# Kernel tuning notes

Measured on AMD Instinct MI355X. Metric: run time of the kernel, lower is better.

Reference implementation:

```python
import jax, jax.numpy as jnp
import numpy as np

BN_EPS = 1e-5
DIST_EPS = 1e-8


def setup_inputs() -> dict:
    key = jax.random.key(0)
    ks = jax.random.split(key, 8)
    B, N, S = 8, 8192, 2048
    D_unk, D_kn = 128, 256
    inp = {
        "unknown_xyz": jax.random.uniform(ks[0], (B, N, 3), dtype=jnp.float32),
        "known_xyz": jax.random.uniform(ks[1], (B, S, 3), dtype=jnp.float32),
        "unknown_points": jax.random.normal(ks[2], (B, N, D_unk), dtype=jnp.float32),
        "known_points": jax.random.normal(ks[3], (B, S, D_kn), dtype=jnp.float32),
        "W0": jax.random.normal(ks[4], (256, 384), dtype=jnp.float32) * (1.0 / np.sqrt(384)),
        "b0": jnp.zeros((256,), jnp.float32),
        "g0": jnp.ones((256,), jnp.float32),
        "beta0": jnp.zeros((256,), jnp.float32),
        "W1": jax.random.normal(ks[5], (128, 256), dtype=jnp.float32) * (1.0 / np.sqrt(256)),
        "b1": jnp.zeros((128,), jnp.float32),
        "g1": jnp.ones((128,), jnp.float32),
        "beta1": jnp.zeros((128,), jnp.float32),
    }
    return inp


def _three_nn(unknown_xyz, known_xyz):
    # squared pairwise distances [B, N, S]
    d = jnp.sum((unknown_xyz[:, :, None, :] - known_xyz[:, None, :, :]) ** 2, axis=-1)
    neg_top, idx = jax.lax.top_k(-d, 3)  # 3 smallest distances
    return -neg_top, idx  # dists [B,N,3], idx [B,N,3]


def _conv_bn_relu(x, W, b, g, beta):
    # x: [B, N, Cin]; 1x1 Conv1d == per-point linear
    y = jnp.einsum("bnc,oc->bno", x, W) + b
    mean = jnp.mean(y, axis=(0, 1))
    var = jnp.var(y, axis=(0, 1))  # biased, as BatchNorm training forward
    y = g * (y - mean) * jax.lax.rsqrt(var + BN_EPS) + beta
    return jax.nn.relu(y)


def reference(unknown_xyz, known_xyz, unknown_points, known_points,
              W0, b0, g0, beta0, W1, b1, g1, beta1):
    dists, idx = _three_nn(unknown_xyz, known_xyz)
    dist_recip = 1.0 / (dists + DIST_EPS)
    weight = dist_recip / jnp.sum(dist_recip, axis=2, keepdims=True)  # [B,N,3]
    # gather 3 neighbor features: [B,N,3,D_kn]
    gathered = jax.vmap(lambda f, i: f[i])(known_points, idx)
    interpolated = jnp.sum(weight[..., None] * gathered, axis=2)  # [B,N,D_kn]
    x = jnp.concatenate([unknown_points, interpolated], axis=-1)  # [B,N,384]
    x = _conv_bn_relu(x, W0, b0, g0, beta0)
    x = _conv_bn_relu(x, W1, b1, g1, beta1)
    return x  # [B, N, 128]
```

## Files before the change

kernel.cpp:

```cpp
#include <hip/hip_runtime.h>
#include <hip/hip_bf16.h>


typedef __attribute__((ext_vector_type(8))) short short8;
typedef __attribute__((ext_vector_type(4))) float f32x4;

#define BB 8
#define NN 8192
#define SS 2048
#define M_TOT (BB * NN)
#define N1DIM 256
#define K2DIM 256
#define N2DIM 128
#define NCH 8
#define CHS (SS / NCH)
#define BK 64

#define KEY_MASK 0xFFFFF800u
#define IDX_MASK 0x7FFu

__device__ __forceinline__ unsigned short f2bf(float f) {
    unsigned int x = __float_as_uint(f);
    unsigned int r = x + 0x7fffu + ((x >> 16) & 1u);
    return (unsigned short)(r >> 16);
}
__device__ __forceinline__ float bf2f(unsigned short u) {
    return __uint_as_float(((unsigned int)u) << 16);
}
__device__ __forceinline__ unsigned int med3_u32(unsigned int a, unsigned int b,
                                                 unsigned int c) {
    unsigned int r;
    asm("v_med3_u32 %0, %1, %2, %3" : "=v"(r) : "v"(a), "v"(b), "v"(c));
    return r;
}

__device__ __forceinline__ void gload_lds16(const void* g, void* lds) {
    __builtin_amdgcn_global_load_lds(
        (const __attribute__((address_space(1))) unsigned int*)g,
        (__attribute__((address_space(3))) unsigned int*)lds, 16, 0, 0);
}

__global__ __launch_bounds__(256) void nn_cand_kernel(
    const float* __restrict__ uxyz,
    const float4* __restrict__ kpack,
    unsigned int* __restrict__ cand)
{
    const int tid  = threadIdx.x;
    const int bid  = blockIdx.x;
    const int ch   = bid & 7;
    const int tile = (bid >> 3) & 31;
    const int b    = bid >> 8;

    const int n = tile * 256 + tid;
    const float* up = uxyz + ((size_t)b * NN + n) * 3;
    const float ux = up[0], uy = up[1], uz = up[2];
    const float uu  = fmaf(ux, ux, fmaf(uy, uy, uz * uz));
    const float m2x = -2.0f * ux, m2y = -2.0f * uy, m2z = -2.0f * uz;

    const float4* kb = kpack + (size_t)b * SS + ch * CHS;
    const int base = ch * CHS;

    unsigned int k0 = 0xFFFFFFFFu, k1 = 0xFFFFFFFFu, k2 = 0xFFFFFFFFu;
#pragma unroll 8
    for (int s = 0; s < CHS; ++s) {
        float4 kc = kb[s];
        float d = kc.w + uu;
        d = fmaf(m2z, kc.z, d);
        d = fmaf(m2y, kc.y, d);
        d = fmaf(m2x, kc.x, d);
        d = fmaxf(d, 0.0f);
        unsigned int key = (__float_as_uint(d) & KEY_MASK) | (unsigned int)(base + s);
        unsigned int nk1 = med3_u32(k0, k1, key);
        unsigned int nk2 = med3_u32(k1, k2, key);
        k0 = min(k0, key);
        k1 = nk1;
        k2 = nk2;
    }

    const size_t pt = (size_t)b * NN + n;
    cand[(size_t)(ch * 3 + 0) * M_TOT + pt] = k0;
    cand[(size_t)(ch * 3 + 1) * M_TOT + pt] = k1;
    cand[(size_t)(ch * 3 + 2) * M_TOT + pt] = k2;
}

__global__ __launch_bounds__(256) void cvt_w_kernel(
    const float* __restrict__ W0, const float* __restrict__ W1,
    const float* __restrict__ kxyz,
    unsigned short* __restrict__ Wa, unsigned short* __restrict__ Wb,
    unsigned short* __restrict__ Wb1, float4* __restrict__ kpack,
    float* __restrict__ statsF)
{
    int i = blockIdx.x * 256 + threadIdx.x;
    if (blockIdx.x == 0) {
        for (int j = threadIdx.x; j < 768; j += 256) statsF[j] = 0.0f;
    }
    if (i < 256 * 384) {
        int o = i / 384, c = i - o * 384;
        unsigned short v = f2bf(W0[i]);
        if (c < 128) Wa[o * 128 + c] = v;
        else         Wb[o * 256 + (c - 128)] = v;
    }
    if (i < N2DIM * K2DIM) Wb1[i] = f2bf(W1[i]);
    if (i < BB * SS) {
        const float* p = kxyz + (size_t)i * 3;
        float px = p[0], py = p[1], pz = p[2];
        kpack[i] = make_float4(px, py, pz, fmaf(px, px, fmaf(py, py, pz * pz)));
    }
}

__global__ __launch_bounds__(512, 4) void zgemm_kernel(
    const float* __restrict__ kpts,
    const unsigned short* __restrict__ Wb,
    unsigned short* __restrict__ Z)
{
    __shared__ __align__(128) unsigned char smem[2 * 32768];

    const int tid = threadIdx.x;
    const int l = tid & 63, w = tid >> 6;
    const int wm = w >> 2, wn = w & 3;
    const int mt = blockIdx.x >> 1, nh = blockIdx.x & 1;
    const int row0 = mt * 128;
    const int srow = l >> 3, sbo = (l & 7) * 16;
    const int lr = tid >> 2, lcq = tid & 3;

    f32x4 acc[4][2];
#pragma unroll
    for (int m = 0; m < 4; ++m)
#pragma unroll
        for (int n = 0; n < 2; ++n) {
            f32x4 z = {0.f, 0.f, 0.f, 0.f};
            acc[m][n] = z;
        }

    const unsigned char* Bb = (const unsigned char*)Wb + (size_t)nh * 128 * 512;
    float4 af0, af1, af2, af3;

    auto issueA = [&](int t) {
        const float* src = kpts + (size_t)(row0 + lr) * 256 + t * 64 + lcq * 16;
        af0 = ((const float4*)src)[0];
        af1 = ((const float4*)src)[1];
        af2 = ((const float4*)src)[2];
        af3 = ((const float4*)src)[3];
    };
    auto stageB = [&](int buf, int t) {
        unsigned char* Bl = smem + buf * 32768 + 16384;
#pragma unroll
        for (int i = 0; i < 2; ++i) {
            const int r = w * 16 + i * 8 + srow;
            gload_lds16(Bb + (size_t)r * 512 + t * 128 + (sbo ^ ((r & 7) << 4)),
                        Bl + r * 128 + sbo);
        }
    };
    auto xformA = [&](int buf) {
        unsigned char* Al = smem + buf * 32768;
        short8 o0, o1;
        o0[0] = (short)f2bf(af0.x); o0[1] = (short)f2bf(af0.y);
        o0[2] = (short)f2bf(af0.z); o0[3] = (short)f2bf(af0.w);
        o0[4] = (short)f2bf(af1.x); o0[5] = (short)f2bf(af1.y);
        o0[6] = (short)f2bf(af1.z); o0[7] = (short)f2bf(af1.w);
        o1[0] = (short)f2bf(af2.x); o1[1] = (short)f2bf(af2.y);
        o1[2] = (short)f2bf(af2.z); o1[3] = (short)f2bf(af2.w);
        o1[4] = (short)f2bf(af3.x); o1[5] = (short)f2bf(af3.y);
        o1[6] = (short)f2bf(af3.z); o1[7] = (short)f2bf(af3.w);
        const int bo = lcq * 32;
        *(short8*)(Al + lr * 128 + ((bo) ^ ((lr & 7) << 4))) = o0;
        *(short8*)(Al + lr * 128 + ((bo + 16) ^ ((lr & 7) << 4))) = o1;
    };
    auto compute = [&](int buf) {
        const unsigned char* Al = smem + buf * 32768;
        const unsigned char* Bl = Al + 16384;
#pragma unroll
        for (int ks = 0; ks < 2; ++ks) {
            const int bo = ks * 64 + (l >> 4) * 16;
            short8 a[4], bq[2];
#pragma unroll
            for (int m = 0; m < 4; ++m) {
                const int r = wm * 64 + m * 16 + (l & 15);
                a[m] = *(const short8*)(Al + r * 128 + (bo ^ ((r & 7) << 4)));
            }
#pragma unroll
            for (int n = 0; n < 2; ++n) {
                const int r = wn * 32 + n * 16 + (l & 15);
                bq[n] = *(const short8*)(Bl + r * 128 + (bo ^ ((r & 7) << 4)));
            }
#pragma unroll
            for (int m = 0; m < 4; ++m)
#pragma unroll
                for (int n = 0; n < 2; ++n)
                    acc[m][n] = __builtin_amdgcn_mfma_f32_16x16x32_bf16(
                        a[m], bq[n], acc[m][n], 0, 0, 0);
        }
    };

    issueA(0);
    stageB(0, 0);
    xformA(0);
    __syncthreads();
#pragma unroll
    for (int t = 0; t < 4; ++t) {
        const int cur = t & 1;
        if (t + 1 < 4) { issueA(t + 1); stageB(cur ^ 1, t + 1); }
        compute(cur);
        if (t + 1 < 4) xformA(cur ^ 1);
        __syncthreads();
    }

#pragma unroll
    for (int m = 0; m < 4; ++m) {
        const int row = row0 + wm * 64 + m * 16 + (l >> 4) * 4;
#pragma unroll
        for (int n = 0; n < 2; ++n) {
            const int col = nh * 128 + wn * 32 + n * 16 + (l & 15);
            f32x4 v = acc[m][n];
#pragma unroll
            for (int r = 0; r < 4; ++r)
                Z[(size_t)(row + r) * 256 + col] = f2bf(v[r]);
        }
    }
}

__global__ __launch_bounds__(256) void merge_interp_z_kernel(
    const unsigned int* __restrict__ cand,
    const float4* __restrict__ kpack,
    const float* __restrict__ uxyz,
    const unsigned short* __restrict__ Z,
    unsigned short* __restrict__ xz)
{
    __shared__ int   sidx[64][3];
    __shared__ float sw[64][3];

    const int tid = threadIdx.x;
    const int bid = blockIdx.x;
    const int b   = bid & 7;
    const int pn  = (bid >> 3) * 64;

    if (tid < 64) {
        const size_t pt = (size_t)b * NN + pn + tid;

        unsigned int k[6];
#pragma unroll
        for (int i = 0; i < 6; ++i) k[i] = 0xFFFFFFFFu;
#pragma unroll
        for (int ch = 0; ch < NCH; ++ch) {
#pragma unroll
            for (int j = 0; j < 3; ++j) {
                unsigned int t = cand[(size_t)(ch * 3 + j) * M_TOT + pt];
#pragma unroll
                for (int i = 0; i < 6; ++i) {
                    unsigned int a = min(k[i], t);
                    t = max(k[i], t);
                    k[i] = a;
                }
            }
        }

        const float* up = uxyz + pt * 3;
        const float ux = up[0], uy = up[1], uz = up[2];
        const float4* kpb4 = kpack + (size_t)b * SS;
        unsigned long long e[6];
#pragma unroll
        for (int i = 0; i < 6; ++i) {
            unsigned int idx = k[i] & IDX_MASK;
            float4 kc = kpb4[idx];
            float dx = kc.x - ux, dy = kc.y - uy, dz = kc.z - uz;
            float d = fmaf(dx, dx, fmaf(dy, dy, dz * dz));
            e[i] = ((unsigned long long)__float_as_uint(d) << 32) | idx;
        }
#pragma unroll
        for (int i = 0; i < 3; ++i)
#pragma unroll
            for (int j = i + 1; j < 6; ++j)
                if (e[j] < e[i]) { unsigned long long t = e[i]; e[i] = e[j]; e[j] = t; }

        float d0 = __uint_as_float((unsigned int)(e[0] >> 32));
        float d1 = __uint_as_float((unsigned int)(e[1] >> 32));
        float d2 = __uint_as_float((unsigned int)(e[2] >> 32));
        float r0 = 1.0f / (d0 + 1e-8f);
        float r1 = 1.0f / (d1 + 1e-8f);
        float r2 = 1.0f / (d2 + 1e-8f);
        float rs = 1.0f / (r0 + r1 + r2);
        sidx[tid][0] = (int)(e[0] & IDX_MASK);
        sidx[tid][1] = (int)(e[1] & IDX_MASK);
        sidx[tid][2] = (int)(e[2] & IDX_MASK);
        sw[tid][0] = r0 * rs; sw[tid][1] = r1 * rs; sw[tid][2] = r2 * rs;
    }
    __syncthreads();

    const int wv = tid >> 6, lane = tid & 63;
    const unsigned short* Zb = Z + (size_t)b * SS * 256;
    for (int p = wv; p < 64; p += 4) {
        const int j0 = sidx[p][0], j1 = sidx[p][1], j2 = sidx[p][2];
        const float w0 = sw[p][0], w1 = sw[p][1], w2 = sw[p][2];

        ushort4 z0 = *(const ushort4*)(Zb + (size_t)j0 * 256 + lane * 4);
        ushort4 z1 = *(const ushort4*)(Zb + (size_t)j1 * 256 + lane * 4);
        ushort4 z2 = *(const ushort4*)(Zb + (size_t)j2 * 256 + lane * 4);
        ushort4 o;
        o.x = f2bf(fmaf(w2, bf2f(z2.x), fmaf(w1, bf2f(z1.x), w0 * bf2f(z0.x))));
        o.y = f2bf(fmaf(w2, bf2f(z2.y), fmaf(w1, bf2f(z1.y), w0 * bf2f(z0.y))));
        o.z = f2bf(fmaf(w2, bf2f(z2.z), fmaf(w1, bf2f(z1.z), w0 * bf2f(z0.z))));
        o.w = f2bf(fmaf(w2, bf2f(z2.w), fmaf(w1, bf2f(z1.w), w0 * bf2f(z0.w))));
        *(ushort4*)(xz + ((size_t)b * NN + pn + p) * 256 + lane * 4) = o;
    }
}

__global__ __launch_bounds__(512, 4) void gemm1z_kernel(
    const float* __restrict__ upts,
    const unsigned short* __restrict__ Wa,
    const unsigned short* __restrict__ xz,
    unsigned short* __restrict__ Y0,
    float* __restrict__ stats)
{
    __shared__ __align__(128) unsigned char smem[65536];

    const int tid = threadIdx.x;
    const int l = tid & 63, w = tid >> 6;
    const int wm = w >> 2, wn = w & 3;
    const int mt = blockIdx.x >> 1, nh = blockIdx.x & 1;
    const int row0 = mt * 128;
    const int srow = l >> 3, sbo = (l & 7) * 16;
    const int lr = tid >> 2, lcq = tid & 3;

    {
        const unsigned char* Bb = (const unsigned char*)Wa + (size_t)nh * 128 * 256;
#pragma unroll
        for (int h = 0; h < 2; ++h)
#pragma unroll
            for (int i = 0; i < 2; ++i) {
                const int r = w * 16 + i * 8 + srow;
                gload_lds16(Bb + (size_t)r * 256 + h * 128 + (sbo ^ ((r & 7) << 4)),
                            smem + 32768 + h * 16384 + r * 128 + sbo);
            }
    }
    {
        const float* src = upts + (size_t)(row0 + lr) * 128 + lcq * 32;
        float4 f[8];
#pragma unroll
        for (int q = 0; q < 8; ++q) f[q] = ((const float4*)src)[q];
        unsigned char* Ah = smem + (lcq >> 1) * 16384;
        const int cb = (lcq & 1) * 64;
#pragma unroll
        for (int q = 0; q < 4; ++q) {
            float4 fa = f[q * 2], fb = f[q * 2 + 1];
            short8 o;
            o[0] = (short)f2bf(fa.x); o[1] = (short)f2bf(fa.y);
            o[2] = (short)f2bf(fa.z); o[3] = (short)f2bf(fa.w);
            o[4] = (short)f2bf(fb.x); o[5] = (short)f2bf(fb.y);
            o[6] = (short)f2bf(fb.z); o[7] = (short)f2bf(fb.w);
            *(short8*)(Ah + lr * 128 + ((cb + q * 16) ^ ((lr & 7) << 4))) = o;
        }
    }
    __syncthreads();

    f32x4 acc[4][2];
#pragma unroll
    for (int m = 0; m < 4; ++m)
#pragma unroll
        for (int n = 0; n < 2; ++n) {
            f32x4 z = {0.f, 0.f, 0.f, 0.f};
            acc[m][n] = z;
        }
#pragma unroll
    for (int ks = 0; ks < 4; ++ks) {
        const unsigned char* Al = smem + (ks >> 1) * 16384;
        const unsigned char* Bl = smem + 32768 + (ks >> 1) * 16384;
        const int bo = (ks & 1) * 64 + (l >> 4) * 16;
        short8 a[4], bq[2];
#pragma unroll
        for (int m = 0; m < 4; ++m) {
            const int r = wm * 64 + m * 16 + (l & 15);
            a[m] = *(const short8*)(Al + r * 128 + (bo ^ ((r & 7) << 4)));
        }
#pragma unroll
        for (int n = 0; n < 2; ++n) {
            const int r = wn * 32 + n * 16 + (l & 15);
            bq[n] = *(const short8*)(Bl + r * 128 + (bo ^ ((r & 7) << 4)));
        }
#pragma unroll
        for (int m = 0; m < 4; ++m)
#pragma unroll
            for (int n = 0; n < 2; ++n)
                acc[m][n] = __builtin_amdgcn_mfma_f32_16x16x32_bf16(
                    a[m], bq[n], acc[m][n], 0, 0, 0);
    }

    float s1[2] = {0.f, 0.f}, s2[2] = {0.f, 0.f};
#pragma unroll
    for (int m = 0; m < 4; ++m) {
#pragma unroll
        for (int r = 0; r < 4; ++r) {
            const int row = row0 + wm * 64 + m * 16 + (l >> 4) * 4 + r;
#pragma unroll
            for (int n = 0; n < 2; ++n) {
                const int col = nh * 128 + wn * 32 + n * 16 + (l & 15);
                float f = acc[m][n][r] + bf2f(xz[(size_t)row * 256 + col]);
                Y0[(size_t)row * 256 + col] = f2bf(f);
                s1[n] += f;
                s2[n] += f * f;
            }
        }
    }
#pragma unroll
    for (int n = 0; n < 2; ++n) {
        s1[n] += __shfl_xor(s1[n], 16, 64);
        s1[n] += __shfl_xor(s1[n], 32, 64);
        s2[n] += __shfl_xor(s2[n], 16, 64);
        s2[n] += __shfl_xor(s2[n], 32, 64);
    }
    if (l < 16) {
#pragma unroll
        for (int n = 0; n < 2; ++n) {
            const int col = nh * 128 + wn * 32 + n * 16 + l;
            atomicAdd(&stats[col], s1[n]);
            atomicAdd(&stats[N1DIM + col], s2[n]);
        }
    }
}

#define G2_NT (K2DIM / BK)
__global__ __launch_bounds__(512, 4) void gemm2_kernel(
    const unsigned short* __restrict__ Y0,
    const unsigned short* __restrict__ Wb,
    const float* __restrict__ stats0,
    const float* __restrict__ g0,
    const float* __restrict__ beta0,
    unsigned short* __restrict__ Y1,
    float* __restrict__ stats)
{
    __shared__ __align__(128) unsigned char smem[2 * 32768];
    __shared__ float sgm[K2DIM], sga[K2DIM];

    const int tid = threadIdx.x;
    const int l = tid & 63, w = tid >> 6;
    const int wm = w >> 2, wn = w & 3;
    const int row0 = blockIdx.x * 128;
    const int srow = l >> 3;
    const int sbo  = (l & 7) * 16;
    const int lr  = tid >> 2;
    const int lcq = tid & 3;

    f32x4 acc[4][2];
#pragma unroll
    for (int m = 0; m < 4; ++m)
#pragma unroll
        for (int n = 0; n < 2; ++n) {
            f32x4 z = {0.f, 0.f, 0.f, 0.f};
            acc[m][n] = z;
        }

    const unsigned char* Bb = (const unsigned char*)Wb;
    short8 areg0, areg1;

    auto issueA = [&](int t) {
        const unsigned short* src = Y0 + (size_t)(row0 + lr) * K2DIM + t * BK + lcq * 16;
        areg0 = *(const short8*)src;
        areg1 = *(const short8*)(src + 8);
    };
    auto stageB = [&](int buf, int t) {
        unsigned char* Bl = smem + buf * 32768 + 16384;
        const int k0b = t * (BK * 2);
#pragma unroll
        for (int i = 0; i < 2; ++i) {
            const int r = w * 16 + i * 8 + srow;
            gload_lds16(Bb + (size_t)r * (K2DIM * 2) + k0b + (sbo ^ ((r & 7) << 4)),
                        Bl + r * 128 + sbo);
        }
    };
    auto xformA = [&](int buf, int t) {
        unsigned char* Al = smem + buf * 32768;
        const int kb = t * BK + lcq * 16;
        short8 o0, o1;
#pragma unroll
        for (int j = 0; j < 8; ++j) {
            float f = bf2f((unsigned short)areg0[j]);
            f = fmaxf(fmaf(f, sgm[kb + j], sga[kb + j]), 0.f);
            o0[j] = (short)f2bf(f);
            float g = bf2f((unsigned short)areg1[j]);
            g = fmaxf(fmaf(g, sgm[kb + 8 + j], sga[kb + 8 + j]), 0.f);
            o1[j] = (short)f2bf(g);
        }
        const int bo = lcq * 32;
        *(short8*)(Al + lr * 128 + ((bo) ^ ((lr & 7) << 4))) = o0;
        *(short8*)(Al + lr * 128 + ((bo + 16) ^ ((lr & 7) << 4))) = o1;
    };
    auto compute = [&](int buf) {
        const unsigned char* Al = smem + buf * 32768;
        const unsigned char* Bl = Al + 16384;
#pragma unroll
        for (int ks = 0; ks < 2; ++ks) {
            const int bo = ks * 64 + (l >> 4) * 16;
            short8 a[4], bq[2];
#pragma unroll
            for (int m = 0; m < 4; ++m) {
                const int r = wm * 64 + m * 16 + (l & 15);
                a[m] = *(const short8*)(Al + r * 128 + (bo ^ ((r & 7) << 4)));
            }
#pragma unroll
            for (int n = 0; n < 2; ++n) {
                const int r = wn * 32 + n * 16 + (l & 15);
                bq[n] = *(const short8*)(Bl + r * 128 + (bo ^ ((r & 7) << 4)));
            }
#pragma unroll
            for (int m = 0; m < 4; ++m)
#pragma unroll
                for (int n = 0; n < 2; ++n)
                    acc[m][n] = __builtin_amdgcn_mfma_f32_16x16x32_bf16(
                        a[m], bq[n], acc[m][n], 0, 0, 0);
        }
    };

    if (tid < K2DIM) {
        const float inv = 1.0f / (float)M_TOT;
        float mean = stats0[tid] * inv;
        float var  = stats0[N1DIM + tid] * inv - mean * mean;
        float m = g0[tid] * rsqrtf(var + 1e-5f);
        sgm[tid] = m;
        sga[tid] = beta0[tid] - mean * m;
    }
    issueA(0);
    stageB(0, 0);
    __syncthreads();
    xformA(0, 0);
    __syncthreads();

#pragma unroll
    for (int t = 0; t < G2_NT; ++t) {
        const int cur = t & 1;
        if (t + 1 < G2_NT) { issueA(t + 1); stageB(cur ^ 1, t + 1); }
        compute(cur);
        if (t + 1 < G2_NT) xformA(cur ^ 1, t + 1);
        __syncthreads();
    }

    float s1[2] = {0.f, 0.f}, s2[2] = {0.f, 0.f};
#pragma unroll
    for (int m = 0; m < 4; ++m) {
        const int row = row0 + wm * 64 + m * 16 + (l >> 4) * 4;
#pragma unroll
        for (int n = 0; n < 2; ++n) {
            const int col = wn * 32 + n * 16 + (l & 15);
            f32x4 v = acc[m][n];
#pragma unroll
            for (int r = 0; r < 4; ++r) {
                float f = v[r];
                Y1[(size_t)(row + r) * N2DIM + col] = f2bf(f);
                s1[n] += f;
                s2[n] += f * f;
            }
        }
    }
#pragma unroll
    for (int n = 0; n < 2; ++n) {
        s1[n] += __shfl_xor(s1[n], 16, 64);
        s1[n] += __shfl_xor(s1[n], 32, 64);
        s2[n] += __shfl_xor(s2[n], 16, 64);
        s2[n] += __shfl_xor(s2[n], 32, 64);
    }
    if (l < 16) {
#pragma unroll
        for (int n = 0; n < 2; ++n) {
            const int col = wn * 32 + n * 16 + l;
            atomicAdd(&stats[col], s1[n]);
            atomicAdd(&stats[N2DIM + col], s2[n]);
        }
    }
}

__global__ __launch_bounds__(256) void bn_out_kernel(
    const unsigned short* __restrict__ Y1, const float* __restrict__ stats1,
    const float* __restrict__ g1, const float* __restrict__ beta1,
    float* __restrict__ out)
{
    __shared__ float sgm[N2DIM], sga[N2DIM];
    const int tid = threadIdx.x;
    if (tid < N2DIM) {
        const float inv = 1.0f / (float)M_TOT;
        float mean = stats1[tid] * inv;
        float var  = stats1[N2DIM + tid] * inv - mean * mean;
        float m = g1[tid] * rsqrtf(var + 1e-5f);
        sgm[tid] = m;
        sga[tid] = beta1[tid] - mean * m;
    }
    __syncthreads();

    const int total = M_TOT * N2DIM / 8;
    for (int i = blockIdx.x * 256 + tid; i < total; i += gridDim.x * 256) {
        short8 v = ((const short8*)Y1)[i];
        const int cg = (i & 15) * 8;
        float4 o1, o2;
        o1.x = fmaxf(fmaf(bf2f((unsigned short)v[0]), sgm[cg + 0], sga[cg + 0]), 0.f);
        o1.y = fmaxf(fmaf(bf2f((unsigned short)v[1]), sgm[cg + 1], sga[cg + 1]), 0.f);
        o1.z = fmaxf(fmaf(bf2f((unsigned short)v[2]), sgm[cg + 2], sga[cg + 2]), 0.f);
        o1.w = fmaxf(fmaf(bf2f((unsigned short)v[3]), sgm[cg + 3], sga[cg + 3]), 0.f);
        o2.x = fmaxf(fmaf(bf2f((unsigned short)v[4]), sgm[cg + 4], sga[cg + 4]), 0.f);
        o2.y = fmaxf(fmaf(bf2f((unsigned short)v[5]), sgm[cg + 5], sga[cg + 5]), 0.f);
        o2.z = fmaxf(fmaf(bf2f((unsigned short)v[6]), sgm[cg + 6], sga[cg + 6]), 0.f);
        o2.w = fmaxf(fmaf(bf2f((unsigned short)v[7]), sgm[cg + 7], sga[cg + 7]), 0.f);
        ((float4*)out)[i * 2]     = o1;
        ((float4*)out)[i * 2 + 1] = o2;
    }
}

extern "C" void kernel_launch(void* const* d_in, const int* in_sizes, int n_in,
                              void* d_out, int out_size, void* d_ws, size_t ws_size,
                              hipStream_t stream)
{
    const float* uxyz  = (const float*)d_in[0];
    const float* kxyz  = (const float*)d_in[1];
    const float* upts  = (const float*)d_in[2];
    const float* kpts  = (const float*)d_in[3];
    const float* W0    = (const float*)d_in[4];
    const float* g0    = (const float*)d_in[6];
    const float* beta0 = (const float*)d_in[7];
    const float* W1    = (const float*)d_in[8];
    const float* g1    = (const float*)d_in[10];
    const float* beta1 = (const float*)d_in[11];
    float* out = (float*)d_out;

    char* ws = (char*)d_ws;
    const size_t off_xz = 0;
    const size_t off_y0 = 33554432;
    const size_t off_z  = 67108864;
    const size_t off_w  = 75497472;

    unsigned short* xz   = (unsigned short*)(ws + off_xz);
    unsigned short* y1   = (unsigned short*)(ws + off_xz);
    unsigned short* y0   = (unsigned short*)(ws + off_y0);
    unsigned int*   cand = (unsigned int*)(ws + off_y0);
    float4*         kpack = (float4*)(ws + off_y0 + 8388608);
    unsigned short* Zb   = (unsigned short*)(ws + off_z);
    unsigned short* wa   = (unsigned short*)(ws + off_w);
    unsigned short* wb   = (unsigned short*)(ws + off_w + 65536);
    unsigned short* wb1  = (unsigned short*)(ws + off_w + 196608);
    float* F = (float*)(ws + off_w + 262144);
    float* stats0 = F;
    float* stats1 = F + 512;

    cvt_w_kernel<<<384, 256, 0, stream>>>(W0, W1, kxyz, wa, wb, wb1, kpack, F);
    nn_cand_kernel<<<2048, 256, 0, stream>>>(uxyz, kpack, cand);
    zgemm_kernel<<<256, 512, 0, stream>>>(kpts, wb, Zb);
    merge_interp_z_kernel<<<1024, 256, 0, stream>>>(cand, kpack, uxyz, Zb, xz);
    gemm1z_kernel<<<1024, 512, 0, stream>>>(upts, wa, xz, y0, stats0);
    gemm2_kernel<<<512, 512, 0, stream>>>(y0, wb1, stats0, g0, beta0, y1, stats1);
    bn_out_kernel<<<2048, 256, 0, stream>>>(y1, stats1, g1, beta1, out);
}
```

Measured before the change: 155.4 us.

## Replace brute-force three-NN search with uniform grid binning plus brute fallback

Known points are scattered into a 5x5x5 uniform grid per batch, with a fixed 32 slots per cell and an atomic counter. Each query scans the 2x2x2 cell block nearest to it, using four lanes and merging their top-5 lists with shuffles. It then checks whether the third-nearest distance is within the block's covered radius. Queries that fail this check, or that touch an overflowed cell, are appended to a list and rescanned by a wave-per-query brute-force kernel. This removes most of the full S=2048 distance scan per query, at the cost of extra kernels, atomics, table initialisation and a fallback whose cost depends on the point distribution.

```diff
diff --git a/kernel.cpp b/kernel.cpp
--- a/kernel.cpp
+++ b/kernel.cpp
@@ -12,9 +12,12 @@
 #define N1DIM 256
 #define K2DIM 256
 #define N2DIM 128
-#define NCH 8
-#define CHS (SS / NCH)
 #define BK 64
+
+#define GDIM 5
+#define NCELL (GDIM * GDIM * GDIM)
+#define SLOTS 32
+#define CELLW 0.2f
 
 #define KEY_MASK 0xFFFFF800u
 #define IDX_MASK 0x7FFu
@@ -34,53 +37,57 @@
     return r;
 }
 
+__device__ __forceinline__ void ins5(unsigned int k[5], unsigned int key) {
+    unsigned int n1 = med3_u32(k[0], k[1], key);
+    unsigned int n2 = med3_u32(k[1], k[2], key);
+    unsigned int n3 = med3_u32(k[2], k[3], key);
+    unsigned int n4 = med3_u32(k[3], k[4], key);
+    k[0] = min(k[0], key);
+    k[1] = n1; k[2] = n2; k[3] = n3; k[4] = n4;
+}
+
+__device__ __forceinline__ float rescue_write(
+    const unsigned int k[5], float qx, float qy, float qz,
+    const float4* __restrict__ kpB, uint4* __restrict__ widx, size_t pt)
+{
+    unsigned long long e[5];
+#pragma unroll
+    for (int i = 0; i < 5; ++i) {
+        if ((k[i] & KEY_MASK) >= 0x7F800000u) {
+            e[i] = 0xFFFFFFFFFFFFFFFFull;
+        } else {
+            unsigned int idx = k[i] & IDX_MASK;
+            float4 c = kpB[idx];
+            float dx = c.x - qx, dy = c.y - qy, dz = c.z - qz;
+            float d = fmaf(dx, dx, fmaf(dy, dy, dz * dz));
+            e[i] = ((unsigned long long)__float_as_uint(d) << 32) | idx;
+        }
+    }
+#pragma unroll
+    for (int i = 0; i < 3; ++i)
+#pragma unroll
+        for (int j = i + 1; j < 5; ++j)
+            if (e[j] < e[i]) { unsigned long long t = e[i]; e[i] = e[j]; e[j] = t; }
+
+    float d0 = __uint_as_float((unsigned int)(e[0] >> 32));
+    float d1 = __uint_as_float((unsigned int)(e[1] >> 32));
+    float d2 = __uint_as_float((unsigned int)(e[2] >> 32));
+    float r0 = 1.0f / (d0 + 1e-8f);
+    float r1 = 1.0f / (d1 + 1e-8f);
+    float r2 = 1.0f / (d2 + 1e-8f);
+    float rs = 1.0f / (r0 + r1 + r2);
+    unsigned int i0 = (unsigned int)(e[0] & IDX_MASK);
+    unsigned int i1 = (unsigned int)(e[1] & IDX_MASK);
+    unsigned int i2 = (unsigned int)(e[2] & IDX_MASK);
+    widx[pt] = make_uint4(__float_as_uint(r0 * rs), __float_as_uint(r1 * rs),
+                          i0 | (i1 << 16), i2);
+    return d2;
+}
+
 __device__ __forceinline__ void gload_lds16(const void* g, void* lds) {
     __builtin_amdgcn_global_load_lds(
         (const __attribute__((address_space(1))) unsigned int*)g,
         (__attribute__((address_space(3))) unsigned int*)lds, 16, 0, 0);
-}
-
-__global__ __launch_bounds__(256) void nn_cand_kernel(
-    const float* __restrict__ uxyz,
-    const float4* __restrict__ kpack,
-    unsigned int* __restrict__ cand)
-{
-    const int tid  = threadIdx.x;
-    const int bid  = blockIdx.x;
-    const int ch   = bid & 7;
-    const int tile = (bid >> 3) & 31;
-    const int b    = bid >> 8;
-
-    const int n = tile * 256 + tid;
-    const float* up = uxyz + ((size_t)b * NN + n) * 3;
-    const float ux = up[0], uy = up[1], uz = up[2];
-    const float uu  = fmaf(ux, ux, fmaf(uy, uy, uz * uz));
-    const float m2x = -2.0f * ux, m2y = -2.0f * uy, m2z = -2.0f * uz;
-
-    const float4* kb = kpack + (size_t)b * SS + ch * CHS;
-    const int base = ch * CHS;
-
-    unsigned int k0 = 0xFFFFFFFFu, k1 = 0xFFFFFFFFu, k2 = 0xFFFFFFFFu;
-#pragma unroll 8
-    for (int s = 0; s < CHS; ++s) {
-        float4 kc = kb[s];
-        float d = kc.w + uu;
-        d = fmaf(m2z, kc.z, d);
-        d = fmaf(m2y, kc.y, d);
-        d = fmaf(m2x, kc.x, d);
-        d = fmaxf(d, 0.0f);
-        unsigned int key = (__float_as_uint(d) & KEY_MASK) | (unsigned int)(base + s);
-        unsigned int nk1 = med3_u32(k0, k1, key);
-        unsigned int nk2 = med3_u32(k1, k2, key);
-        k0 = min(k0, key);
-        k1 = nk1;
-        k2 = nk2;
-    }
-
-    const size_t pt = (size_t)b * NN + n;
-    cand[(size_t)(ch * 3 + 0) * M_TOT + pt] = k0;
-    cand[(size_t)(ch * 3 + 1) * M_TOT + pt] = k1;
-    cand[(size_t)(ch * 3 + 2) * M_TOT + pt] = k2;
 }
 
 __global__ __launch_bounds__(256) void cvt_w_kernel(
@@ -88,12 +95,17 @@
     const float* __restrict__ kxyz,
     unsigned short* __restrict__ Wa, unsigned short* __restrict__ Wb,
     unsigned short* __restrict__ Wb1, float4* __restrict__ kpack,
-    float* __restrict__ statsF)
+    float4* __restrict__ table, int* __restrict__ cnt,
+    int* __restrict__ nfail, float* __restrict__ statsF)
 {
     int i = blockIdx.x * 256 + threadIdx.x;
     if (blockIdx.x == 0) {
         for (int j = threadIdx.x; j < 768; j += 256) statsF[j] = 0.0f;
-    }
+        if (threadIdx.x == 0) *nfail = 0;
+    }
+    if (i < BB * NCELL) cnt[i] = 0;
+    if (i < BB * NCELL * SLOTS)
+        table[i] = make_float4(1e30f, 1e30f, 1e30f, 0.0f);
     if (i < 256 * 384) {
         int o = i / 384, c = i - o * 384;
         unsigned short v = f2bf(W0[i]);
@@ -105,6 +117,141 @@
         const float* p = kxyz + (size_t)i * 3;
         float px = p[0], py = p[1], pz = p[2];
         kpack[i] = make_float4(px, py, pz, fmaf(px, px, fmaf(py, py, pz * pz)));
+    }
+}
+
+__global__ __launch_bounds__(256) void bin_scatter_kernel(
+    const float* __restrict__ kxyz, float4* __restrict__ table,
+    int* __restrict__ cnt)
+{
+    int i = blockIdx.x * 256 + threadIdx.x;
+    if (i >= BB * SS) return;
+    int b = i >> 11, s = i & 2047;
+    const float* p = kxyz + (size_t)i * 3;
+    float x = p[0], y = p[1], z = p[2];
+    int cx = min((int)(x * GDIM), GDIM - 1);
+    int cy = min((int)(y * GDIM), GDIM - 1);
+    int cz = min((int)(z * GDIM), GDIM - 1);
+    int cell = (cz * GDIM + cy) * GDIM + cx;
+    int slot = atomicAdd(&cnt[b * NCELL + cell], 1);
+    if (slot < SLOTS)
+        table[((size_t)(b * NCELL + cell)) * SLOTS + slot] =
+            make_float4(x, y, z, __int_as_float(s));
+}
+
+__global__ __launch_bounds__(256) void nn_grid_kernel(
+    const float* __restrict__ uxyz, const float4* __restrict__ table,
+    const int* __restrict__ cnt, const float4* __restrict__ kpack,
+    uint4* __restrict__ widx, int* __restrict__ fail_list,
+    int* __restrict__ nfail)
+{
+    const int t  = blockIdx.x * 256 + threadIdx.x;
+    const int qd = t & 3;
+    const size_t pt = (size_t)(t >> 2);
+    const int b = (int)(pt >> 13);
+
+    const float* up = uxyz + pt * 3;
+    const float qx = up[0], qy = up[1], qz = up[2];
+
+    const int cx = min((int)(qx * GDIM), GDIM - 1);
+    const int cy = min((int)(qy * GDIM), GDIM - 1);
+    const int cz = min((int)(qz * GDIM), GDIM - 1);
+    const float fx = qx * GDIM - cx, fy = qy * GDIM - cy, fz = qz * GDIM - cz;
+    int ox = cx - (fx <= 0.5f ? 1 : 0); ox = max(0, min(ox, GDIM - 2));
+    int oy = cy - (fy <= 0.5f ? 1 : 0); oy = max(0, min(oy, GDIM - 2));
+    int oz = cz - (fz <= 0.5f ? 1 : 0); oz = max(0, min(oz, GDIM - 2));
+
+    const float4* tb = table + (size_t)b * NCELL * SLOTS;
+    const int* cb = cnt + b * NCELL;
+
+    unsigned int k[5] = {0xFFFFFFFFu, 0xFFFFFFFFu, 0xFFFFFFFFu,
+                         0xFFFFFFFFu, 0xFFFFFFFFu};
+    int ovf = 0;
+#pragma unroll
+    for (int jj = 0; jj < 2; ++jj) {
+        const int j = qd * 2 + jj;
+        const int dx = j & 1, dy = (j >> 1) & 1, dz = j >> 2;
+        const int cell = ((oz + dz) * GDIM + (oy + dy)) * GDIM + (ox + dx);
+        ovf |= (cb[cell] > SLOTS) ? 1 : 0;
+        const float4* cp = tb + (size_t)cell * SLOTS;
+#pragma unroll 8
+        for (int s = 0; s < SLOTS; ++s) {
+            float4 c = cp[s];
+            float ddx = c.x - qx, ddy = c.y - qy, ddz = c.z - qz;
+            float d = fmaf(ddx, ddx, fmaf(ddy, ddy, ddz * ddz));
+            unsigned int key = (__float_as_uint(d) & KEY_MASK) |
+                               (unsigned int)__float_as_int(c.w);
+            ins5(k, key);
+        }
+    }
+
+#pragma unroll
+    for (int m = 1; m <= 2; m <<= 1) {
+        unsigned int f0 = (unsigned int)__shfl_xor((int)k[0], m);
+        unsigned int f1 = (unsigned int)__shfl_xor((int)k[1], m);
+        unsigned int f2 = (unsigned int)__shfl_xor((int)k[2], m);
+        unsigned int f3 = (unsigned int)__shfl_xor((int)k[3], m);
+        unsigned int f4 = (unsigned int)__shfl_xor((int)k[4], m);
+        ovf |= __shfl_xor(ovf, m);
+        ins5(k, f0); ins5(k, f1); ins5(k, f2); ins5(k, f3); ins5(k, f4);
+    }
+
+    if (qd != 0) return;
+
+    float d3 = rescue_write(k, qx, qy, qz, kpack + (size_t)b * SS, widx, pt);
+
+    float lx = ox * CELLW, rx = (ox + 2) * CELLW;
+    float ly = oy * CELLW, ry = (oy + 2) * CELLW;
+    float lz = oz * CELLW, rz = (oz + 2) * CELLW;
+    float covx = fminf(ox == 0 ? 1e30f : qx - lx, ox == GDIM - 2 ? 1e30f : rx - qx);
+    float covy = fminf(oy == 0 ? 1e30f : qy - ly, oy == GDIM - 2 ? 1e30f : ry - qy);
+    float covz = fminf(oz == 0 ? 1e30f : qz - lz, oz == GDIM - 2 ? 1e30f : rz - qz);
+    float g = fminf(covx, fminf(covy, covz));
+
+    if (ovf || !(d3 <= g * g)) {
+        int pos = atomicAdd(nfail, 1);
+        fail_list[pos] = (int)pt;
+    }
+}
+
+__global__ __launch_bounds__(256) void nn_brute_kernel(
+    const float* __restrict__ uxyz, const float4* __restrict__ kpack,
+    const int* __restrict__ fail_list, const int* __restrict__ nfail,
+    uint4* __restrict__ widx)
+{
+    const int l = threadIdx.x & 63;
+    const int wv = (blockIdx.x * 256 + threadIdx.x) >> 6;
+    const int nw = (gridDim.x * 256) >> 6;
+    const int n = *nfail;
+
+    for (int q = wv; q < n; q += nw) {
+        const size_t pt = (size_t)fail_list[q];
+        const int b = (int)(pt >> 13);
+        const float* up = uxyz + pt * 3;
+        const float qx = up[0], qy = up[1], qz = up[2];
+        const float4* kp = kpack + (size_t)b * SS;
+
+        unsigned int k[5] = {0xFFFFFFFFu, 0xFFFFFFFFu, 0xFFFFFFFFu,
+                             0xFFFFFFFFu, 0xFFFFFFFFu};
+#pragma unroll 4
+        for (int s = l; s < SS; s += 64) {
+            float4 c = kp[s];
+            float ddx = c.x - qx, ddy = c.y - qy, ddz = c.z - qz;
+            float d = fmaf(ddx, ddx, fmaf(ddy, ddy, ddz * ddz));
+            unsigned int key = (__float_as_uint(d) & KEY_MASK) | (unsigned int)s;
+            ins5(k, key);
+        }
+#pragma unroll
+        for (int m = 1; m <= 32; m <<= 1) {
+            unsigned int f0 = (unsigned int)__shfl_xor((int)k[0], m);
+            unsigned int f1 = (unsigned int)__shfl_xor((int)k[1], m);
+            unsigned int f2 = (unsigned int)__shfl_xor((int)k[2], m);
+            unsigned int f3 = (unsigned int)__shfl_xor((int)k[3], m);
+            unsigned int f4 = (unsigned int)__shfl_xor((int)k[4], m);
+            ins5(k, f0); ins5(k, f1); ins5(k, f2); ins5(k, f3); ins5(k, f4);
+        }
+        if (l == 0)
+            rescue_write(k, qx, qy, qz, kp, widx, pt);
     }
 }
 
@@ -219,10 +366,8 @@
     }
 }
 
-__global__ __launch_bounds__(256) void merge_interp_z_kernel(
-    const unsigned int* __restrict__ cand,
-    const float4* __restrict__ kpack,
-    const float* __restrict__ uxyz,
+__global__ __launch_bounds__(256) void interp_z_kernel(
+    const uint4* __restrict__ widx,
     const unsigned short* __restrict__ Z,
     unsigned short* __restrict__ xz)
 {
@@ -235,60 +380,19 @@
     const int pn  = (bid >> 3) * 64;
 
     if (tid < 64) {
-        const size_t pt = (size_t)b * NN + pn + tid;
-
-        unsigned int k[6];
-#pragma unroll
-        for (int i = 0; i < 6; ++i) k[i] = 0xFFFFFFFFu;
-#pragma unroll
-        for (int ch = 0; ch < NCH; ++ch) {
-#pragma unroll
-            for (int j = 0; j < 3; ++j) {
-                unsigned int t = cand[(size_t)(ch * 3 + j) * M_TOT + pt];
-#pragma unroll
-                for (int i = 0; i < 6; ++i) {
-                    unsigned int a = min(k[i], t);
-                    t = max(k[i], t);
-                    k[i] = a;
-                }
-            }
-        }
-
-        const float* up = uxyz + pt * 3;
-        const float ux = up[0], uy = up[1], uz = up[2];
-        const float4* kpb4 = kpack + (size_t)b * SS;
-        unsigned long long e[6];
-#pragma unroll
-        for (int i = 0; i < 6; ++i) {
-            unsigned int idx = k[i] & IDX_MASK;
-            float4 kc = kpb4[idx];
-            float dx = kc.x - ux, dy = kc.y - uy, dz = kc.z - uz;
-            float d = fmaf(dx, dx, fmaf(dy, dy, dz * dz));
-            e[i] = ((unsigned long long)__float_as_uint(d) << 32) | idx;
-        }
-#pragma unroll
-        for (int i = 0; i < 3; ++i)
-#pragma unroll
-            for (int j = i + 1; j < 6; ++j)
-                if (e[j] < e[i]) { unsigned long long t = e[i]; e[i] = e[j]; e[j] = t; }
-
-        float d0 = __uint_as_float((unsigned int)(e[0] >> 32));
-        float d1 = __uint_as_float((unsigned int)(e[1] >> 32));
-        float d2 = __uint_as_float((unsigned int)(e[2] >> 32));
-        float r0 = 1.0f / (d0 + 1e-8f);
-        float r1 = 1.0f / (d1 + 1e-8f);
-        float r2 = 1.0f / (d2 + 1e-8f);
-        float rs = 1.0f / (r0 + r1 + r2);
-        sidx[tid][0] = (int)(e[0] & IDX_MASK);
-        sidx[tid][1] = (int)(e[1] & IDX_MASK);
-        sidx[tid][2] = (int)(e[2] & IDX_MASK);
-        sw[tid][0] = r0 * rs; sw[tid][1] = r1 * rs; sw[tid][2] = r2 * rs;
+        uint4 wv = widx[(size_t)b * NN + pn + tid];
+        float w0 = __uint_as_float(wv.x);
+        float w1 = __uint_as_float(wv.y);
+        sidx[tid][0] = (int)(wv.z & 0xFFFFu);
+        sidx[tid][1] = (int)(wv.z >> 16);
+        sidx[tid][2] = (int)wv.w;
+        sw[tid][0] = w0; sw[tid][1] = w1; sw[tid][2] = 1.0f - w0 - w1;
     }
     __syncthreads();
 
-    const int wv = tid >> 6, lane = tid & 63;
+    const int wvv = tid >> 6, lane = tid & 63;
     const unsigned short* Zb = Z + (size_t)b * SS * 256;
-    for (int p = wv; p < 64; p += 4) {
+    for (int p = wvv; p < 64; p += 4) {
         const int j0 = sidx[p][0], j1 = sidx[p][1], j2 = sidx[p][2];
         const float w0 = sw[p][0], w1 = sw[p][1], w2 = sw[p][2];
 
@@ -626,8 +730,11 @@
     unsigned short* xz   = (unsigned short*)(ws + off_xz);
     unsigned short* y1   = (unsigned short*)(ws + off_xz);
     unsigned short* y0   = (unsigned short*)(ws + off_y0);
-    unsigned int*   cand = (unsigned int*)(ws + off_y0);
-    float4*         kpack = (float4*)(ws + off_y0 + 8388608);
+    float4* table    = (float4*)(ws + off_y0);
+    int*    cellcnt  = (int*)(ws + off_y0 + 524288);
+    int*    nfail    = (int*)(ws + off_y0 + 528384);
+    int*    faillist = (int*)(ws + off_y0 + 532480);
+    float4* kpack    = (float4*)(ws + off_y0 + 8388608);
     unsigned short* Zb   = (unsigned short*)(ws + off_z);
     unsigned short* wa   = (unsigned short*)(ws + off_w);
     unsigned short* wb   = (unsigned short*)(ws + off_w + 65536);
@@ -635,11 +742,16 @@
     float* F = (float*)(ws + off_w + 262144);
     float* stats0 = F;
     float* stats1 = F + 512;
-
-    cvt_w_kernel<<<384, 256, 0, stream>>>(W0, W1, kxyz, wa, wb, wb1, kpack, F);
-    nn_cand_kernel<<<2048, 256, 0, stream>>>(uxyz, kpack, cand);
+    uint4* widx = (uint4*)(ws + off_w + 270336);
+
+    cvt_w_kernel<<<384, 256, 0, stream>>>(W0, W1, kxyz, wa, wb, wb1, kpack,
+                                          table, cellcnt, nfail, F);
+    bin_scatter_kernel<<<64, 256, 0, stream>>>(kxyz, table, cellcnt);
+    nn_grid_kernel<<<1024, 256, 0, stream>>>(uxyz, table, cellcnt, kpack,
+                                             widx, faillist, nfail);
+    nn_brute_kernel<<<256, 256, 0, stream>>>(uxyz, kpack, faillist, nfail, widx);
     zgemm_kernel<<<256, 512, 0, stream>>>(kpts, wb, Zb);
-    merge_interp_z_kernel<<<1024, 256, 0, stream>>>(cand, kpack, uxyz, Zb, xz);
+    interp_z_kernel<<<1024, 256, 0, stream>>>(widx, Zb, xz);
     gemm1z_kernel<<<1024, 512, 0, stream>>>(upts, wa, xz, y0, stats0);
     gemm2_kernel<<<512, 512, 0, stream>>>(y0, wb1, stats0, g0, beta0, y1, stats1);
     bn_out_kernel<<<2048, 256, 0, stream>>>(y1, stats1, g1, beta1, out);
```

Result: slower. 162.8 us (+4.8%).
